# Kernel tuning notes

Hardware: AMD Instinct MI355X
Metric: run time of the kernel (lower is better)

The kernel has to match this reference:

```python
import jax, jax.numpy as jnp
import numpy as np

B, S, H = 64, 512, 256
H2 = 2 * H
TOPK, TRUNC = 5, 100
EPS = 1e-7
TMAX = S + 1  # h_old slot 0 is the initial zero state; one slot appended per step
NEG = -1e9


def setup_inputs() -> dict:
    key = jax.random.key(0)
    ks = jax.random.split(key, 8)
    p = lambda k, shape: jax.random.normal(k, shape, jnp.float32) * 0.08
    return {
        "x": jax.random.normal(ks[0], (B, S), jnp.float32),
        "W_ih_f": p(ks[1], (4 * H, 1)),
        "W_hh_f": p(ks[2], (4 * H, H)),
        "b_f": p(ks[3], (4 * H,)),
        "W_ih_b": p(ks[4], (4 * H, 1)),
        "W_hh_b": p(ks[5], (4 * H, H)),
        "b_b": p(ks[6], (4 * H,)),
        "w_t": p(ks[7], (4 * H, 1)),
    }


def _lstm_cell(xt, h, c, W_ih, W_hh, b):
    # torch.nn.LSTMCell: gates ordered i, f, g, o
    g = xt @ W_ih.T + h @ W_hh.T + b
    i, f, gg, o = jnp.split(g, 4, axis=1)
    i, f, o = jax.nn.sigmoid(i), jax.nn.sigmoid(f), jax.nn.sigmoid(o)
    c2 = f * c + i * jnp.tanh(gg)
    return o * jnp.tanh(c2), c2


def _forward(x, W_ih_f, W_hh_f, b_f, W_ih_b, W_hh_b, b_b, w_t):
    # tanh(cat(h_comb, h_old)) @ w_t == tanh(h_comb)@w1 + tanh(h_old)@w2
    w1, w2 = w_t[:H2, 0], w_t[H2:, 0]
    pos = jnp.arange(TMAX)

    h0 = jnp.zeros((B, H), jnp.float32)
    h_old0 = jnp.zeros((B, TMAX, H2), jnp.float32)   # slot 0 = initial zeros (valid)
    th_old0 = jnp.zeros((B, TMAX, H2), jnp.float32)  # cached tanh(h_old)
    carry0 = (h0, h0, h0, h0, h_old0, th_old0,
              jnp.zeros((B, H2), jnp.float32), jnp.zeros((B, TMAX), jnp.float32))

    def step(carry, i):
        h_f, c_f, h_b, c_b, h_old, th_old, _, _ = carry
        trunc = ((i + 1) % TRUNC) == 0  # TBPTT detach point
        sg = lambda a: jnp.where(trunc, jax.lax.stop_gradient(a), a)
        h_f, c_f, h_b, c_b = sg(h_f), sg(c_f), sg(h_b), sg(c_b)

        xf = jax.lax.dynamic_slice_in_dim(x, i, 1, axis=1)          # [B,1]
        xb = jax.lax.dynamic_slice_in_dim(x, S - 1 - i, 1, axis=1)  # [B,1]
        h_f, c_f = _lstm_cell(xf, h_f, c_f, W_ih_f, W_hh_f, b_f)
        h_b, c_b = _lstm_cell(xb, h_b, c_b, W_ih_b, W_hh_b, b_b)
        h_comb = jnp.concatenate([h_f, h_b], axis=1)  # [B,2H]

        rs = i + 1                    # remember_size before append
        valid = pos < rs              # [TMAX]
        s = jnp.tanh(h_comb) @ w1[:, None] + th_old @ w2  # [B,1]+[B,TMAX]
        s_m = jnp.where(valid[None, :], s, NEG)

        # Sparse_attention: subtract k-th largest, clamp at 0, renormalize
        delta = jax.lax.top_k(s_m, TOPK)[0][:, -1] + EPS  # [B]
        w_sp = jnp.clip(s_m - delta[:, None], 0.0, None)
        w_sp = w_sp / (w_sp.sum(axis=1, keepdims=True) + EPS)
        w_raw = jnp.where(valid[None, :], s, 0.0)  # time_step <= top_k branch
        attn_w = jnp.where(rs <= TOPK, w_raw, w_sp)  # [B,TMAX]

        attn_c = jnp.einsum('bt,bth->bh', attn_w, h_old)  # weighted sum of cache
        h_new = h_comb + attn_c

        h_old = jax.lax.dynamic_update_slice_in_dim(
            h_old, h_new[:, None, :], i + 1, axis=1)
        th_old = jax.lax.dynamic_update_slice_in_dim(
            th_old, jnp.tanh(h_new)[:, None, :], i + 1, axis=1)
        return (h_f, c_f, h_b, c_b, h_old, th_old, attn_c, attn_w), None

    carry, _ = jax.lax.scan(step, carry0, jnp.arange(S))
    attn_c, attn_w = carry[6], carry[7]
    # last step: remember_size == S, torch returns [B, S, 1]
    return attn_c, attn_w[:, :S, None]


def reference(x, W_ih_f, W_hh_f, b_f, W_ih_b, W_hh_b, b_b, w_t):
    return _forward(x, W_ih_f, W_hh_f, b_f, W_ih_b, W_hh_b, b_b, w_t)
```

## Files before the change

kernel.cpp:

```cpp
#include <hip/hip_runtime.h>
#include <math.h>

#define BB    64
#define SS    512
#define HH    256
#define HH2   512
#define TMAXX 513
#define NTOP  5
#define EPSF  1e-7f

#if defined(__has_builtin)
#if __has_builtin(__builtin_amdgcn_sdot4)
#define HAVE_SDOT4 1
#endif
#endif

__device__ __forceinline__ int dot4i8_(unsigned a, int b, int c) {
#ifdef HAVE_SDOT4
  return __builtin_amdgcn_sdot4((int)a, b, c, false);
#else
  int acc = c;
#pragma unroll
  for (int j = 0; j < 4; ++j) {
    int av = (int)(signed char)(a >> (8 * j));
    int bv = (int)(signed char)(((unsigned)b) >> (8 * j));
    acc += av * bv;
  }
  return acc;
#endif
}

__device__ __forceinline__ float dpp_sum64(float x) {
  int t;
  t = __builtin_amdgcn_update_dpp(0, __builtin_bit_cast(int, x), 0x111, 0xf, 0xf, true);
  x += __builtin_bit_cast(float, t);
  t = __builtin_amdgcn_update_dpp(0, __builtin_bit_cast(int, x), 0x112, 0xf, 0xf, true);
  x += __builtin_bit_cast(float, t);
  t = __builtin_amdgcn_update_dpp(0, __builtin_bit_cast(int, x), 0x114, 0xf, 0xe, true);
  x += __builtin_bit_cast(float, t);
  t = __builtin_amdgcn_update_dpp(0, __builtin_bit_cast(int, x), 0x118, 0xf, 0xc, true);
  x += __builtin_bit_cast(float, t);
  t = __builtin_amdgcn_update_dpp(0, __builtin_bit_cast(int, x), 0x142, 0xa, 0xf, true);
  x += __builtin_bit_cast(float, t);
  t = __builtin_amdgcn_update_dpp(0, __builtin_bit_cast(int, x), 0x143, 0xc, 0xf, true);
  x += __builtin_bit_cast(float, t);
  return __builtin_bit_cast(float, __builtin_amdgcn_readlane(__builtin_bit_cast(int, x), 63));
}


__global__ void init_kernel(const float* __restrict__ Whh_f, const float* __restrict__ Whh_b,
                            uint4* __restrict__ wq, float* __restrict__ scales) {
  int t = blockIdx.x * blockDim.x + threadIdx.x;
  if (t >= 2048) return;
  int d = t >> 10, row = t & 1023;
  const float* src = (d ? Whh_b : Whh_f) + (size_t)row * HH;
  float m = 1e-20f;
  for (int k = 0; k < HH; ++k) m = fmaxf(m, fabsf(src[k]));
  float inv = 127.f / m;
  scales[t] = m * (1.f / 16129.f);
  for (int kq4 = 0; kq4 < 16; ++kq4) {
    unsigned u[4];
#pragma unroll
    for (int w = 0; w < 4; ++w) {
      unsigned uu = 0;
#pragma unroll
      for (int j = 0; j < 4; ++j) {
        float q = rintf(src[kq4 * 16 + w * 4 + j] * inv);
        q = fminf(fmaxf(q, -127.f), 127.f);
        uu |= ((unsigned)(((int)q) & 0xff)) << (8 * j);
      }
      u[w] = uu;
    }
    wq[(size_t)(d * 16 + kq4) * 1024 + row] = make_uint4(u[0], u[1], u[2], u[3]);
  }
}

__global__ __launch_bounds__(1024, 4)
void lstm_kernel(const float* __restrict__ x,
                 const float* __restrict__ wihf, const float* __restrict__ bf,
                 const float* __restrict__ wihb, const float* __restrict__ bb_,
                 const uint4* __restrict__ wq, const float* __restrict__ scales,
                 float* __restrict__ hcomb) {
  const int r    = blockIdx.x >> 1;
  const int d    = blockIdx.x & 1;
  const int tid  = threadIdx.x;
  const int gate = tid >> 8;
  const int e    = tid & 255;

  __shared__ float x_lds[SS];
  __shared__ float gact[1024];
  __shared__ int   hbuf[2][64];

  for (int t = tid; t < SS; t += 1024) x_lds[t] = x[(size_t)r * SS + t];
  if (tid < 64) hbuf[0][tid] = 0;

  const float wihv = d ? wihb[tid] : wihf[tid];
  const float bv   = d ? bb_[tid]  : bf[tid];
  const float sc   = scales[d * 1024 + tid];

  uint4 w[16];
  {
    const uint4* wb = wq + (size_t)(d * 16) * 1024 + tid;
#pragma unroll
    for (int q = 0; q < 16; ++q) w[q] = wb[(size_t)q * 1024];
  }
#pragma unroll
  for (int q = 0; q < 16; ++q)
    asm volatile("" : "+v"(w[q].x), "+v"(w[q].y), "+v"(w[q].z), "+v"(w[q].w));

  float c = 0.f;
  float* hout = hcomb + (size_t)r * SS * HH2 + d * HH;
  __syncthreads();

  int cur = 0;
  for (int i = 0; i < SS; ++i) {
    const int4* hp = (const int4*)hbuf[cur];
    int a = 0;
#pragma unroll
    for (int q = 0; q < 16; ++q) {
      int4 h4 = hp[q];
      a = dot4i8_(w[q].x, h4.x, a);
      a = dot4i8_(w[q].y, h4.y, a);
      a = dot4i8_(w[q].z, h4.z, a);
      a = dot4i8_(w[q].w, h4.w, a);
    }
    float xv = x_lds[d ? (SS - 1 - i) : i];
    float gv = (float)a * sc + fmaf(xv, wihv, bv);
    gact[tid] = (gate == 2) ? tanhf(gv) : 1.f / (1.f + expf(-gv));
    __syncthreads();
    float ig = gact[e];
    float fg = gact[HH + e];
    float gg = gact[2 * HH + e];
    float og = gact[3 * HH + e];
    c = fg * c + ig * gg;
    float hn = og * tanhf(c);
    if (gate == 0) {
      hout[(size_t)i * HH2 + e] = hn;
      ((signed char*)hbuf[cur ^ 1])[e] = (signed char)(int)rintf(hn * 127.f);
    }
    cur ^= 1;
    __syncthreads();
  }
}

__global__ __launch_bounds__(64, 1)
void attn_kernel(const float* __restrict__ w_t, const float* __restrict__ hcomb,
                 float* __restrict__ out) {
  const int b = blockIdx.x;
  const int l = threadIdx.x;
  const float* hrow = hcomb + (size_t)b * SS * HH2;

  __shared__ float tw_l[TMAXX];

  const float4 w1a = *(const float4*)(w_t + 4 * l);
  const float4 w1b = *(const float4*)(w_t + HH + 4 * l);
  const float4 w2a = *(const float4*)(w_t + HH2 + 4 * l);
  const float4 w2b = *(const float4*)(w_t + HH2 + HH + 4 * l);

  float t5v[5] = {0.f, -1e30f, -1e30f, -1e30f, -1e30f};
  int   t5s[5] = {0, 1, 2, 3, 4};
  int   t5cnt  = 1;
  float4 z4 = make_float4(0.f, 0.f, 0.f, 0.f);
  float4 sA0 = z4, sA1 = z4, sA2 = z4, sA3 = z4, sA4 = z4;
  float4 sB0 = z4, sB1 = z4, sB2 = z4, sB3 = z4, sB4 = z4;
  if (l == 0) tw_l[0] = 0.f;

  float tw5 = 0.f, inv = 0.f;

  float4 a0 = *(const float4*)(hrow + 0 * HH2 + 4 * l);
  float4 b0 = *(const float4*)(hrow + 0 * HH2 + HH + 4 * l);
  float4 a1 = *(const float4*)(hrow + 1 * HH2 + 4 * l);
  float4 b1 = *(const float4*)(hrow + 1 * HH2 + HH + 4 * l);
  float4 a2 = *(const float4*)(hrow + 2 * HH2 + 4 * l);
  float4 b2 = *(const float4*)(hrow + 2 * HH2 + HH + 4 * l);
  float4 a3 = *(const float4*)(hrow + 3 * HH2 + 4 * l);
  float4 b3 = *(const float4*)(hrow + 3 * HH2 + HH + 4 * l);

  auto step = [&](float4& ha, float4& hb, int i) {
    float wr[5];
    if (i >= NTOP) {
      tw5 = t5v[4];
      float rk0 = fmaxf(t5v[0] - tw5 - EPSF, 0.f);
      float rk1 = fmaxf(t5v[1] - tw5 - EPSF, 0.f);
      float rk2 = fmaxf(t5v[2] - tw5 - EPSF, 0.f);
      float rk3 = fmaxf(t5v[3] - tw5 - EPSF, 0.f);
      inv = 1.f / (rk0 + rk1 + rk2 + rk3 + EPSF);
      wr[0] = rk0 * inv; wr[1] = rk1 * inv; wr[2] = rk2 * inv; wr[3] = rk3 * inv;
      wr[4] = 0.f;
    } else {
      float sv = tanhf(ha.x) * w1a.x + tanhf(ha.y) * w1a.y +
                 tanhf(ha.z) * w1a.z + tanhf(ha.w) * w1a.w +
                 tanhf(hb.x) * w1b.x + tanhf(hb.y) * w1b.y +
                 tanhf(hb.z) * w1b.z + tanhf(hb.w) * w1b.w;
      float s = dpp_sum64(sv);
#pragma unroll
      for (int k = 0; k < 5; ++k) wr[k] = (k < t5cnt) ? (s + t5v[k]) : 0.f;
    }
    float ws0 = 0.f, ws1 = 0.f, ws2 = 0.f, ws3 = 0.f, ws4 = 0.f;
#pragma unroll
    for (int k = 0; k < 5; ++k) {
      float wv = wr[k]; int s2 = t5s[k];
      ws0 += (s2 == 0) ? wv : 0.f;
      ws1 += (s2 == 1) ? wv : 0.f;
      ws2 += (s2 == 2) ? wv : 0.f;
      ws3 += (s2 == 3) ? wv : 0.f;
      ws4 += (s2 == 4) ? wv : 0.f;
    }
    float4 cxA, cxB;
    cxA.x = ws0*sA0.x + ws1*sA1.x + ws2*sA2.x + ws3*sA3.x + ws4*sA4.x;
    cxA.y = ws0*sA0.y + ws1*sA1.y + ws2*sA2.y + ws3*sA3.y + ws4*sA4.y;
    cxA.z = ws0*sA0.z + ws1*sA1.z + ws2*sA2.z + ws3*sA3.z + ws4*sA4.z;
    cxA.w = ws0*sA0.w + ws1*sA1.w + ws2*sA2.w + ws3*sA3.w + ws4*sA4.w;
    cxB.x = ws0*sB0.x + ws1*sB1.x + ws2*sB2.x + ws3*sB3.x + ws4*sB4.x;
    cxB.y = ws0*sB0.y + ws1*sB1.y + ws2*sB2.y + ws3*sB3.y + ws4*sB4.y;
    cxB.z = ws0*sB0.z + ws1*sB1.z + ws2*sB2.z + ws3*sB3.z + ws4*sB4.z;
    cxB.w = ws0*sB0.w + ws1*sB1.w + ws2*sB2.w + ws3*sB3.w + ws4*sB4.w;
    float4 hnA, hnB;
    hnA.x = ha.x + cxA.x; hnA.y = ha.y + cxA.y; hnA.z = ha.z + cxA.z; hnA.w = ha.w + cxA.w;
    hnB.x = hb.x + cxB.x; hnB.y = hb.y + cxB.y; hnB.z = hb.z + cxB.z; hnB.w = hb.w + cxB.w;
    float pv = tanhf(hnA.x) * w2a.x + tanhf(hnA.y) * w2a.y +
               tanhf(hnA.z) * w2a.z + tanhf(hnA.w) * w2a.w +
               tanhf(hnB.x) * w2b.x + tanhf(hnB.y) * w2b.y +
               tanhf(hnB.z) * w2b.z + tanhf(hnB.w) * w2b.w;
    float v = dpp_sum64(pv);
    if (l == 0) tw_l[i + 1] = v;
    if (i == SS - 1) {
      *(float4*)(out + (size_t)b * HH2 + 4 * l)      = cxA;
      *(float4*)(out + (size_t)b * HH2 + HH + 4 * l) = cxB;
      float* ow = out + (size_t)BB * HH2 + (size_t)b * SS;
#pragma unroll
      for (int j = 0; j < 8; ++j) {
        int t = j * 64 + l;
        float rr = tw_l[t] - tw5 - EPSF;
        ow[t] = rr > 0.f ? rr * inv : 0.f;
      }
      return;
    }
    bool full = (t5cnt >= 5);
    bool ins  = !full || (v > t5v[4]);
    if (ins) {
      int p    = full ? 4 : t5cnt;
      int slot = full ? t5s[4] : t5cnt;
#pragma unroll
      for (int k = 0; k < 5; ++k) if (k == p) { t5v[k] = v; t5s[k] = slot; }
      if (slot == 0)      { sA0 = hnA; sB0 = hnB; }
      else if (slot == 1) { sA1 = hnA; sB1 = hnB; }
      else if (slot == 2) { sA2 = hnA; sB2 = hnB; }
      else if (slot == 3) { sA3 = hnA; sB3 = hnB; }
      else                { sA4 = hnA; sB4 = hnB; }
      if (!full) ++t5cnt;
#pragma unroll
      for (int k = 4; k >= 1; --k) {
        bool sw = (k <= p) && (t5v[k] > t5v[k - 1]);
        float v0 = t5v[k - 1], v1 = t5v[k];
        int   s0 = t5s[k - 1], s1 = t5s[k];
        t5v[k] = sw ? v0 : v1;  t5v[k - 1] = sw ? v1 : v0;
        t5s[k] = sw ? s0 : s1;  t5s[k - 1] = sw ? s1 : s0;
      }
    }
    if (i + 4 < SS) {
      ha = *(const float4*)(hrow + (size_t)(i + 4) * HH2 + 4 * l);
      hb = *(const float4*)(hrow + (size_t)(i + 4) * HH2 + HH + 4 * l);
    }
  };

  for (int i = 0; i < SS; i += 4) {
    step(a0, b0, i);
    step(a1, b1, i + 1);
    step(a2, b2, i + 2);
    step(a3, b3, i + 3);
  }
}

extern "C" void kernel_launch(void* const* d_in, const int* in_sizes, int n_in,
                              void* d_out, int out_size, void* d_ws, size_t ws_size,
                              hipStream_t stream) {
  const float* x     = (const float*)d_in[0];
  const float* Wih_f = (const float*)d_in[1];
  const float* Whh_f = (const float*)d_in[2];
  const float* b_f   = (const float*)d_in[3];
  const float* Wih_b = (const float*)d_in[4];
  const float* Whh_b = (const float*)d_in[5];
  const float* b_b   = (const float*)d_in[6];
  const float* w_t   = (const float*)d_in[7];
  float* out = (float*)d_out;

  char* ws = (char*)d_ws;
  uint4*  wq     = (uint4*)ws;
  float*  scales = (float*)(ws + (1 << 20));
  float*  hcomb  = (float*)(ws + (4 << 20));

  init_kernel<<<8, 256, 0, stream>>>(Whh_f, Whh_b, wq, scales);
  lstm_kernel<<<2 * BB, 1024, 0, stream>>>(x, Wih_f, b_f, Wih_b, b_b,
                                           wq, scales, hcomb);
  attn_kernel<<<BB, 64, 0, stream>>>(w_t, hcomb, out);
}
```

Measured before the change: 1.356 ms.

## Compute all four LSTM gates per thread and broadcast hidden state via readlane

```diff
diff --git a/kernel.cpp b/kernel.cpp
--- a/kernel.cpp
+++ b/kernel.cpp
@@ -45,6 +45,11 @@
   t = __builtin_amdgcn_update_dpp(0, __builtin_bit_cast(int, x), 0x143, 0xc, 0xf, true);
   x += __builtin_bit_cast(float, t);
   return __builtin_bit_cast(float, __builtin_amdgcn_readlane(__builtin_bit_cast(int, x), 63));
+}
+
+__device__ __forceinline__ float fast_tanh(float x) {
+  float t = exp2f(x * -2.885390082f);
+  return fmaf(__builtin_amdgcn_rcpf(1.f + t), 2.f, -1.f);
 }
 
 
@@ -75,38 +80,47 @@
   }
 }
 
-__global__ __launch_bounds__(1024, 4)
+__global__ __launch_bounds__(256, 1)
 void lstm_kernel(const float* __restrict__ x,
                  const float* __restrict__ wihf, const float* __restrict__ bf,
                  const float* __restrict__ wihb, const float* __restrict__ bb_,
                  const uint4* __restrict__ wq, const float* __restrict__ scales,
                  float* __restrict__ hcomb) {
-  const int r    = blockIdx.x >> 1;
-  const int d    = blockIdx.x & 1;
-  const int tid  = threadIdx.x;
-  const int gate = tid >> 8;
-  const int e    = tid & 255;
+  const int r = blockIdx.x >> 1;
+  const int d = blockIdx.x & 1;
+  const int e = threadIdx.x;
+  const int l = e & 63;
 
   __shared__ float x_lds[SS];
-  __shared__ float gact[1024];
   __shared__ int   hbuf[2][64];
 
-  for (int t = tid; t < SS; t += 1024) x_lds[t] = x[(size_t)r * SS + t];
-  if (tid < 64) hbuf[0][tid] = 0;
-
-  const float wihv = d ? wihb[tid] : wihf[tid];
-  const float bv   = d ? bb_[tid]  : bf[tid];
-  const float sc   = scales[d * 1024 + tid];
-
-  uint4 w[16];
-  {
-    const uint4* wb = wq + (size_t)(d * 16) * 1024 + tid;
-#pragma unroll
-    for (int q = 0; q < 16; ++q) w[q] = wb[(size_t)q * 1024];
-  }
-#pragma unroll
-  for (int q = 0; q < 16; ++q)
-    asm volatile("" : "+v"(w[q].x), "+v"(w[q].y), "+v"(w[q].z), "+v"(w[q].w));
+  for (int t = e; t < SS; t += 256) x_lds[t] = x[(size_t)r * SS + t];
+  if (e < 64) hbuf[0][e] = 0;
+
+  float wih[4], bias[4], sc[4];
+#pragma unroll
+  for (int g = 0; g < 4; ++g) {
+    int row = g * HH + e;
+    wih[g]  = d ? wihb[row] : wihf[row];
+    bias[g] = d ? bb_[row]  : bf[row];
+    sc[g]   = scales[d * 1024 + row];
+  }
+  uint4 w0[16], w1[16], w2[16], w3[16];
+#pragma unroll
+  for (int q = 0; q < 16; ++q) {
+    const uint4* wb = wq + (size_t)(d * 16 + q) * 1024;
+    w0[q] = wb[0 * HH + e];
+    w1[q] = wb[1 * HH + e];
+    w2[q] = wb[2 * HH + e];
+    w3[q] = wb[3 * HH + e];
+  }
+#pragma unroll
+  for (int q = 0; q < 16; ++q) {
+    asm volatile("" : "+v"(w0[q].x), "+v"(w0[q].y), "+v"(w0[q].z), "+v"(w0[q].w));
+    asm volatile("" : "+v"(w1[q].x), "+v"(w1[q].y), "+v"(w1[q].z), "+v"(w1[q].w));
+    asm volatile("" : "+v"(w2[q].x), "+v"(w2[q].y), "+v"(w2[q].z), "+v"(w2[q].w));
+    asm volatile("" : "+v"(w3[q].x), "+v"(w3[q].y), "+v"(w3[q].z), "+v"(w3[q].w));
+  }
 
   float c = 0.f;
   float* hout = hcomb + (size_t)r * SS * HH2 + d * HH;
@@ -114,30 +128,42 @@
 
   int cur = 0;
   for (int i = 0; i < SS; ++i) {
-    const int4* hp = (const int4*)hbuf[cur];
-    int a = 0;
+    int hq = hbuf[cur][l];
+    int hs[64];
+#pragma unroll
+    for (int j = 0; j < 64; ++j) hs[j] = __builtin_amdgcn_readlane(hq, j);
+    int a0 = 0, a1 = 0, a2 = 0, a3 = 0;
 #pragma unroll
     for (int q = 0; q < 16; ++q) {
-      int4 h4 = hp[q];
-      a = dot4i8_(w[q].x, h4.x, a);
-      a = dot4i8_(w[q].y, h4.y, a);
-      a = dot4i8_(w[q].z, h4.z, a);
-      a = dot4i8_(w[q].w, h4.w, a);
+      a0 = dot4i8_(w0[q].x, hs[4 * q + 0], a0);
+      a0 = dot4i8_(w0[q].y, hs[4 * q + 1], a0);
+      a0 = dot4i8_(w0[q].z, hs[4 * q + 2], a0);
+      a0 = dot4i8_(w0[q].w, hs[4 * q + 3], a0);
+      a1 = dot4i8_(w1[q].x, hs[4 * q + 0], a1);
+      a1 = dot4i8_(w1[q].y, hs[4 * q + 1], a1);
+      a1 = dot4i8_(w1[q].z, hs[4 * q + 2], a1);
+      a1 = dot4i8_(w1[q].w, hs[4 * q + 3], a1);
+      a2 = dot4i8_(w2[q].x, hs[4 * q + 0], a2);
+      a2 = dot4i8_(w2[q].y, hs[4 * q + 1], a2);
+      a2 = dot4i8_(w2[q].z, hs[4 * q + 2], a2);
+      a2 = dot4i8_(w2[q].w, hs[4 * q + 3], a2);
+      a3 = dot4i8_(w3[q].x, hs[4 * q + 0], a3);
+      a3 = dot4i8_(w3[q].y, hs[4 * q + 1], a3);
+      a3 = dot4i8_(w3[q].z, hs[4 * q + 2], a3);
+      a3 = dot4i8_(w3[q].w, hs[4 * q + 3], a3);
     }
     float xv = x_lds[d ? (SS - 1 - i) : i];
-    float gv = (float)a * sc + fmaf(xv, wihv, bv);
-    gact[tid] = (gate == 2) ? tanhf(gv) : 1.f / (1.f + expf(-gv));
-    __syncthreads();
-    float ig = gact[e];
-    float fg = gact[HH + e];
-    float gg = gact[2 * HH + e];
-    float og = gact[3 * HH + e];
-    c = fg * c + ig * gg;
+    float gi = (float)a0 * sc[0] + fmaf(xv, wih[0], bias[0]);
+    float gf = (float)a1 * sc[1] + fmaf(xv, wih[1], bias[1]);
+    float gg = (float)a2 * sc[2] + fmaf(xv, wih[2], bias[2]);
+    float go = (float)a3 * sc[3] + fmaf(xv, wih[3], bias[3]);
+    float ig = 1.f / (1.f + expf(-gi));
+    float fg = 1.f / (1.f + expf(-gf));
+    float og = 1.f / (1.f + expf(-go));
+    c = fg * c + ig * tanhf(gg);
     float hn = og * tanhf(c);
-    if (gate == 0) {
-      hout[(size_t)i * HH2 + e] = hn;
-      ((signed char*)hbuf[cur ^ 1])[e] = (signed char)(int)rintf(hn * 127.f);
-    }
+    hout[(size_t)i * HH2 + e] = hn;
+    ((signed char*)hbuf[cur ^ 1])[e] = (signed char)(int)rintf(hn * 127.f);
     cur ^= 1;
     __syncthreads();
   }
@@ -184,14 +210,14 @@
       float rk1 = fmaxf(t5v[1] - tw5 - EPSF, 0.f);
       float rk2 = fmaxf(t5v[2] - tw5 - EPSF, 0.f);
       float rk3 = fmaxf(t5v[3] - tw5 - EPSF, 0.f);
-      inv = 1.f / (rk0 + rk1 + rk2 + rk3 + EPSF);
+      inv = __builtin_amdgcn_rcpf(rk0 + rk1 + rk2 + rk3 + EPSF);
       wr[0] = rk0 * inv; wr[1] = rk1 * inv; wr[2] = rk2 * inv; wr[3] = rk3 * inv;
       wr[4] = 0.f;
     } else {
-      float sv = tanhf(ha.x) * w1a.x + tanhf(ha.y) * w1a.y +
-                 tanhf(ha.z) * w1a.z + tanhf(ha.w) * w1a.w +
-                 tanhf(hb.x) * w1b.x + tanhf(hb.y) * w1b.y +
-                 tanhf(hb.z) * w1b.z + tanhf(hb.w) * w1b.w;
+      float sv = fast_tanh(ha.x) * w1a.x + fast_tanh(ha.y) * w1a.y +
+                 fast_tanh(ha.z) * w1a.z + fast_tanh(ha.w) * w1a.w +
+                 fast_tanh(hb.x) * w1b.x + fast_tanh(hb.y) * w1b.y +
+                 fast_tanh(hb.z) * w1b.z + fast_tanh(hb.w) * w1b.w;
       float s = dpp_sum64(sv);
 #pragma unroll
       for (int k = 0; k < 5; ++k) wr[k] = (k < t5cnt) ? (s + t5v[k]) : 0.f;
@@ -218,10 +244,10 @@
     float4 hnA, hnB;
     hnA.x = ha.x + cxA.x; hnA.y = ha.y + cxA.y; hnA.z = ha.z + cxA.z; hnA.w = ha.w + cxA.w;
     hnB.x = hb.x + cxB.x; hnB.y = hb.y + cxB.y; hnB.z = hb.z + cxB.z; hnB.w = hb.w + cxB.w;
-    float pv = tanhf(hnA.x) * w2a.x + tanhf(hnA.y) * w2a.y +
-               tanhf(hnA.z) * w2a.z + tanhf(hnA.w) * w2a.w +
-               tanhf(hnB.x) * w2b.x + tanhf(hnB.y) * w2b.y +
-               tanhf(hnB.z) * w2b.z + tanhf(hnB.w) * w2b.w;
+    float pv = fast_tanh(hnA.x) * w2a.x + fast_tanh(hnA.y) * w2a.y +
+               fast_tanh(hnA.z) * w2a.z + fast_tanh(hnA.w) * w2a.w +
+               fast_tanh(hnB.x) * w2b.x + fast_tanh(hnB.y) * w2b.y +
+               fast_tanh(hnB.z) * w2b.z + fast_tanh(hnB.w) * w2b.w;
     float v = dpp_sum64(pv);
     if (l == 0) tw_l[i + 1] = v;
     if (i == SS - 1) {
@@ -291,7 +317,7 @@
   float*  hcomb  = (float*)(ws + (4 << 20));
 
   init_kernel<<<8, 256, 0, stream>>>(Whh_f, Whh_b, wq, scales);
-  lstm_kernel<<<2 * BB, 1024, 0, stream>>>(x, Wih_f, b_f, Wih_b, b_b,
-                                           wq, scales, hcomb);
+  lstm_kernel<<<2 * BB, 256, 0, stream>>>(x, Wih_f, b_f, Wih_b, b_b,
+                                          wq, scales, hcomb);
   attn_kernel<<<BB, 64, 0, stream>>>(w_t, hcomb, out);
 }
```

Result: faster. 1.172 ms (-13.6%).

## Halve LSTM block threads with two gate rows per thread, readlane broadcast, fast activations

Applied to the files above, without the earlier changes.

```diff
diff --git a/kernel.cpp b/kernel.cpp
--- a/kernel.cpp
+++ b/kernel.cpp
@@ -45,6 +45,15 @@
   t = __builtin_amdgcn_update_dpp(0, __builtin_bit_cast(int, x), 0x143, 0xc, 0xf, true);
   x += __builtin_bit_cast(float, t);
   return __builtin_bit_cast(float, __builtin_amdgcn_readlane(__builtin_bit_cast(int, x), 63));
+}
+
+__device__ __forceinline__ float fast_tanh(float x) {
+  float t = exp2f(x * -2.885390082f);
+  return fmaf(__builtin_amdgcn_rcpf(1.f + t), 2.f, -1.f);
+}
+__device__ __forceinline__ float fast_sigmoid(float x) {
+  float t = exp2f(x * -1.442695041f);
+  return __builtin_amdgcn_rcpf(1.f + t);
 }
 
 
@@ -75,7 +84,7 @@
   }
 }
 
-__global__ __launch_bounds__(1024, 4)
+__global__ __launch_bounds__(512, 2)
 void lstm_kernel(const float* __restrict__ x,
                  const float* __restrict__ wihf, const float* __restrict__ bf,
                  const float* __restrict__ wihb, const float* __restrict__ bb_,
@@ -84,29 +93,38 @@
   const int r    = blockIdx.x >> 1;
   const int d    = blockIdx.x & 1;
   const int tid  = threadIdx.x;
-  const int gate = tid >> 8;
+  const int half = tid >> 8;
   const int e    = tid & 255;
+  const int l    = tid & 63;
+  const int rowA = half * 512 + e;
+  const int rowB = half * 512 + 256 + e;
 
   __shared__ float x_lds[SS];
   __shared__ float gact[1024];
   __shared__ int   hbuf[2][64];
 
-  for (int t = tid; t < SS; t += 1024) x_lds[t] = x[(size_t)r * SS + t];
+  for (int t = tid; t < SS; t += 512) x_lds[t] = x[(size_t)r * SS + t];
   if (tid < 64) hbuf[0][tid] = 0;
 
-  const float wihv = d ? wihb[tid] : wihf[tid];
-  const float bv   = d ? bb_[tid]  : bf[tid];
-  const float sc   = scales[d * 1024 + tid];
-
-  uint4 w[16];
-  {
-    const uint4* wb = wq + (size_t)(d * 16) * 1024 + tid;
-#pragma unroll
-    for (int q = 0; q < 16; ++q) w[q] = wb[(size_t)q * 1024];
-  }
-#pragma unroll
-  for (int q = 0; q < 16; ++q)
-    asm volatile("" : "+v"(w[q].x), "+v"(w[q].y), "+v"(w[q].z), "+v"(w[q].w));
+  const float wihA = d ? wihb[rowA] : wihf[rowA];
+  const float wihB = d ? wihb[rowB] : wihf[rowB];
+  const float bA   = d ? bb_[rowA]  : bf[rowA];
+  const float bB   = d ? bb_[rowB]  : bf[rowB];
+  const float scA  = scales[d * 1024 + rowA];
+  const float scB  = scales[d * 1024 + rowB];
+
+  uint4 wA[16], wB[16];
+#pragma unroll
+  for (int q = 0; q < 16; ++q) {
+    const uint4* wb = wq + (size_t)(d * 16 + q) * 1024;
+    wA[q] = wb[rowA];
+    wB[q] = wb[rowB];
+  }
+#pragma unroll
+  for (int q = 0; q < 16; ++q) {
+    asm volatile("" : "+v"(wA[q].x), "+v"(wA[q].y), "+v"(wA[q].z), "+v"(wA[q].w));
+    asm volatile("" : "+v"(wB[q].x), "+v"(wB[q].y), "+v"(wB[q].z), "+v"(wB[q].w));
+  }
 
   float c = 0.f;
   float* hout = hcomb + (size_t)r * SS * HH2 + d * HH;
@@ -114,27 +132,37 @@
 
   int cur = 0;
   for (int i = 0; i < SS; ++i) {
-    const int4* hp = (const int4*)hbuf[cur];
-    int a = 0;
+    int hq = hbuf[cur][l];
+    int hs[64];
+#pragma unroll
+    for (int j = 0; j < 64; ++j) hs[j] = __builtin_amdgcn_readlane(hq, j);
+    int aA = 0, aB = 0;
 #pragma unroll
     for (int q = 0; q < 16; ++q) {
-      int4 h4 = hp[q];
-      a = dot4i8_(w[q].x, h4.x, a);
-      a = dot4i8_(w[q].y, h4.y, a);
-      a = dot4i8_(w[q].z, h4.z, a);
-      a = dot4i8_(w[q].w, h4.w, a);
+      aA = dot4i8_(wA[q].x, hs[4 * q + 0], aA);
+      aB = dot4i8_(wB[q].x, hs[4 * q + 0], aB);
+      aA = dot4i8_(wA[q].y, hs[4 * q + 1], aA);
+      aB = dot4i8_(wB[q].y, hs[4 * q + 1], aB);
+      aA = dot4i8_(wA[q].z, hs[4 * q + 2], aA);
+      aB = dot4i8_(wB[q].z, hs[4 * q + 2], aB);
+      aA = dot4i8_(wA[q].w, hs[4 * q + 3], aA);
+      aB = dot4i8_(wB[q].w, hs[4 * q + 3], aB);
     }
     float xv = x_lds[d ? (SS - 1 - i) : i];
-    float gv = (float)a * sc + fmaf(xv, wihv, bv);
-    gact[tid] = (gate == 2) ? tanhf(gv) : 1.f / (1.f + expf(-gv));
+    float gA = (float)aA * scA + fmaf(xv, wihA, bA);
+    float gB = (float)aB * scB + fmaf(xv, wihB, bB);
+    float actA = half ? fast_tanh(gA)    : fast_sigmoid(gA);
+    float actB = fast_sigmoid(gB);
+    gact[half * 512 + e]       = actA;
+    gact[half * 512 + 256 + e] = actB;
     __syncthreads();
-    float ig = gact[e];
-    float fg = gact[HH + e];
-    float gg = gact[2 * HH + e];
-    float og = gact[3 * HH + e];
-    c = fg * c + ig * gg;
-    float hn = og * tanhf(c);
-    if (gate == 0) {
+    if (tid < HH) {
+      float ig = gact[e];
+      float fg = gact[256 + e];
+      float gg = gact[512 + e];
+      float og = gact[768 + e];
+      c = fg * c + ig * gg;
+      float hn = og * fast_tanh(c);
       hout[(size_t)i * HH2 + e] = hn;
       ((signed char*)hbuf[cur ^ 1])[e] = (signed char)(int)rintf(hn * 127.f);
     }
@@ -143,14 +171,15 @@
   }
 }
 
-__global__ __launch_bounds__(64, 1)
+__global__ __launch_bounds__(512, 1)
 void attn_kernel(const float* __restrict__ w_t, const float* __restrict__ hcomb,
                  float* __restrict__ out) {
-  const int b = blockIdx.x;
-  const int l = threadIdx.x;
+  const int wv = threadIdx.x >> 6;
+  const int l  = threadIdx.x & 63;
+  const int b  = blockIdx.x * 8 + wv;
   const float* hrow = hcomb + (size_t)b * SS * HH2;
 
-  __shared__ float tw_l[TMAXX];
+  __shared__ float tw_l[8][TMAXX];
 
   const float4 w1a = *(const float4*)(w_t + 4 * l);
   const float4 w1b = *(const float4*)(w_t + HH + 4 * l);
@@ -163,7 +192,7 @@
   float4 z4 = make_float4(0.f, 0.f, 0.f, 0.f);
   float4 sA0 = z4, sA1 = z4, sA2 = z4, sA3 = z4, sA4 = z4;
   float4 sB0 = z4, sB1 = z4, sB2 = z4, sB3 = z4, sB4 = z4;
-  if (l == 0) tw_l[0] = 0.f;
+  if (l == 0) tw_l[wv][0] = 0.f;
 
   float tw5 = 0.f, inv = 0.f;
 
@@ -184,14 +213,14 @@
       float rk1 = fmaxf(t5v[1] - tw5 - EPSF, 0.f);
       float rk2 = fmaxf(t5v[2] - tw5 - EPSF, 0.f);
       float rk3 = fmaxf(t5v[3] - tw5 - EPSF, 0.f);
-      inv = 1.f / (rk0 + rk1 + rk2 + rk3 + EPSF);
+      inv = __builtin_amdgcn_rcpf(rk0 + rk1 + rk2 + rk3 + EPSF);
       wr[0] = rk0 * inv; wr[1] = rk1 * inv; wr[2] = rk2 * inv; wr[3] = rk3 * inv;
       wr[4] = 0.f;
     } else {
-      float sv = tanhf(ha.x) * w1a.x + tanhf(ha.y) * w1a.y +
-                 tanhf(ha.z) * w1a.z + tanhf(ha.w) * w1a.w +
-                 tanhf(hb.x) * w1b.x + tanhf(hb.y) * w1b.y +
-                 tanhf(hb.z) * w1b.z + tanhf(hb.w) * w1b.w;
+      float sv = fast_tanh(ha.x) * w1a.x + fast_tanh(ha.y) * w1a.y +
+                 fast_tanh(ha.z) * w1a.z + fast_tanh(ha.w) * w1a.w +
+                 fast_tanh(hb.x) * w1b.x + fast_tanh(hb.y) * w1b.y +
+                 fast_tanh(hb.z) * w1b.z + fast_tanh(hb.w) * w1b.w;
       float s = dpp_sum64(sv);
 #pragma unroll
       for (int k = 0; k < 5; ++k) wr[k] = (k < t5cnt) ? (s + t5v[k]) : 0.f;
@@ -199,12 +228,12 @@
     float ws0 = 0.f, ws1 = 0.f, ws2 = 0.f, ws3 = 0.f, ws4 = 0.f;
 #pragma unroll
     for (int k = 0; k < 5; ++k) {
-      float wv = wr[k]; int s2 = t5s[k];
-      ws0 += (s2 == 0) ? wv : 0.f;
-      ws1 += (s2 == 1) ? wv : 0.f;
-      ws2 += (s2 == 2) ? wv : 0.f;
-      ws3 += (s2 == 3) ? wv : 0.f;
-      ws4 += (s2 == 4) ? wv : 0.f;
+      float wvk = wr[k]; int s2 = t5s[k];
+      ws0 += (s2 == 0) ? wvk : 0.f;
+      ws1 += (s2 == 1) ? wvk : 0.f;
+      ws2 += (s2 == 2) ? wvk : 0.f;
+      ws3 += (s2 == 3) ? wvk : 0.f;
+      ws4 += (s2 == 4) ? wvk : 0.f;
     }
     float4 cxA, cxB;
     cxA.x = ws0*sA0.x + ws1*sA1.x + ws2*sA2.x + ws3*sA3.x + ws4*sA4.x;
@@ -218,12 +247,12 @@
     float4 hnA, hnB;
     hnA.x = ha.x + cxA.x; hnA.y = ha.y + cxA.y; hnA.z = ha.z + cxA.z; hnA.w = ha.w + cxA.w;
     hnB.x = hb.x + cxB.x; hnB.y = hb.y + cxB.y; hnB.z = hb.z + cxB.z; hnB.w = hb.w + cxB.w;
-    float pv = tanhf(hnA.x) * w2a.x + tanhf(hnA.y) * w2a.y +
-               tanhf(hnA.z) * w2a.z + tanhf(hnA.w) * w2a.w +
-               tanhf(hnB.x) * w2b.x + tanhf(hnB.y) * w2b.y +
-               tanhf(hnB.z) * w2b.z + tanhf(hnB.w) * w2b.w;
+    float pv = fast_tanh(hnA.x) * w2a.x + fast_tanh(hnA.y) * w2a.y +
+               fast_tanh(hnA.z) * w2a.z + fast_tanh(hnA.w) * w2a.w +
+               fast_tanh(hnB.x) * w2b.x + fast_tanh(hnB.y) * w2b.y +
+               fast_tanh(hnB.z) * w2b.z + fast_tanh(hnB.w) * w2b.w;
     float v = dpp_sum64(pv);
-    if (l == 0) tw_l[i + 1] = v;
+    if (l == 0) tw_l[wv][i + 1] = v;
     if (i == SS - 1) {
       *(float4*)(out + (size_t)b * HH2 + 4 * l)      = cxA;
       *(float4*)(out + (size_t)b * HH2 + HH + 4 * l) = cxB;
@@ -231,7 +260,7 @@
 #pragma unroll
       for (int j = 0; j < 8; ++j) {
         int t = j * 64 + l;
-        float rr = tw_l[t] - tw5 - EPSF;
+        float rr = tw_l[wv][t] - tw5 - EPSF;
         ow[t] = rr > 0.f ? rr * inv : 0.f;
       }
       return;
@@ -291,7 +320,7 @@
   float*  hcomb  = (float*)(ws + (4 << 20));
 
   init_kernel<<<8, 256, 0, stream>>>(Whh_f, Whh_b, wq, scales);
-  lstm_kernel<<<2 * BB, 1024, 0, stream>>>(x, Wih_f, b_f, Wih_b, b_b,
-                                           wq, scales, hcomb);
-  attn_kernel<<<BB, 64, 0, stream>>>(w_t, hcomb, out);
-}
+  lstm_kernel<<<2 * BB, 512, 0, stream>>>(x, Wih_f, b_f, Wih_b, b_b,
+                                          wq, scales, hcomb);
+  attn_kernel<<<8, 512, 0, stream>>>(w_t, hcomb, out);
+}
```

Result: slower. 1.439 ms (+6.1%).
